# Performance work log

Hardware: AMD Instinct MI355X
Metric: run time of the kernel (lower is better)

The kernel has to match this reference:

```python
import jax, jax.numpy as jnp
import numpy as np

NUM_FEATURES = 35
NEG = -1e30  # effective -inf that is safe under exp/log


def setup_inputs() -> dict:
    key = jax.random.key(0)
    k1, k2, k3, k4 = jax.random.split(key, 4)
    B, T, S = 16, 500, 100
    logits = jax.random.normal(k1, (B, T, NUM_FEATURES), dtype=jnp.float32)
    targets = jax.random.randint(k2, (B, S, NUM_FEATURES), 0, 2, dtype=jnp.int32)
    input_lengths = jax.random.randint(k3, (B,), 300, T + 1, dtype=jnp.int32)
    target_lengths = jax.random.randint(k4, (B,), 10, S + 1, dtype=jnp.int32)
    blank_logit = jnp.zeros((1,), dtype=jnp.float32)
    return {"logits": logits, "blank_logit": blank_logit, "targets": targets,
            "input_lengths": input_lengths, "target_lengths": target_lengths}


def _lse3(a, b, c):
    m = jnp.maximum(jnp.maximum(a, b), c)
    return m + jnp.log(jnp.exp(a - m) + jnp.exp(b - m) + jnp.exp(c - m))


def _sctc_sb_loss(logits, blank_logit, targets, input_lengths, target_lengths):
    B, T, Fdim = logits.shape
    S = targets.shape[1]
    E = 2 * S + 1  # extended (blank-interleaved) target length

    # 3-class logits per feature: [absent=-x, present=x, shared blank]
    blank = jnp.broadcast_to(blank_logit.reshape(1, 1, 1), (B, T, Fdim))
    three = jnp.stack([-logits, logits, blank], axis=-1)           # (B,T,F,3)
    logp = jax.nn.log_softmax(three, axis=-1)                       # (B,T,F,3)

    # extended targets: [blank, y0, blank, y1, ..., blank], blank id = 2
    tgt = jnp.transpose(targets, (0, 2, 1))                         # (B,F,S)
    ext = jnp.full((B, Fdim, E), 2, dtype=jnp.int32)
    ext = ext.at[:, :, 1::2].set(tgt)                               # (B,F,E)

    # skip transition allowed if ext[s] != blank and ext[s] != ext[s-2]
    ext_m2 = jnp.pad(ext, ((0, 0), (0, 0), (2, 0)), constant_values=-1)[:, :, :E]
    allow_skip = (ext != 2) & (ext != ext_m2)                       # (B,F,E)

    # gather log-probs of extended labels: (T,B,F,E)
    lpT = jnp.transpose(logp, (1, 0, 2, 3))                         # (T,B,F,3)
    idx = jnp.broadcast_to(ext[None], (T, B, Fdim, E))
    lp_ext = jnp.take_along_axis(lpT, idx, axis=3)                  # (T,B,F,E)

    # alpha init at t=0
    alpha0 = jnp.full((B, Fdim, E), NEG, dtype=logp.dtype)
    alpha0 = alpha0.at[:, :, 0].set(lp_ext[0, :, :, 0])
    alpha0 = alpha0.at[:, :, 1].set(lp_ext[0, :, :, 1])

    def step(alpha, inp):
        lp_t, t = inp
        a1 = jnp.pad(alpha, ((0, 0), (0, 0), (1, 0)), constant_values=NEG)[:, :, :E]
        a2 = jnp.pad(alpha, ((0, 0), (0, 0), (2, 0)), constant_values=NEG)[:, :, :E]
        a2 = jnp.where(allow_skip, a2, NEG)
        new = _lse3(alpha, a1, a2) + lp_t
        active = (t < input_lengths)[:, None, None]
        return jnp.where(active, new, alpha), None

    alpha, _ = jax.lax.scan(step, alpha0, (lp_ext[1:], jnp.arange(1, T)))

    # log-likelihood = lse(alpha[2L], alpha[2L-1]) at final active frame
    L = target_lengths
    i1 = jnp.broadcast_to((2 * L)[:, None, None], (B, Fdim, 1))
    i2 = jnp.broadcast_to((2 * L - 1)[:, None, None], (B, Fdim, 1))
    aL = jnp.take_along_axis(alpha, i1, axis=2)[..., 0]
    aL1 = jnp.take_along_axis(alpha, i2, axis=2)[..., 0]
    m = jnp.maximum(aL, aL1)
    ll = m + jnp.log(jnp.exp(aL - m) + jnp.exp(aL1 - m))
    loss_bf = -ll                                                   # (B,F)
    # zero_infinity=True
    loss_bf = jnp.where(loss_bf > 0.5 * -NEG, 0.0, loss_bf)
    # CTCLoss reduction='mean': divide by target length, mean over batch;
    # then sum over features / NUM_FEATURES == mean over features
    per_bf = loss_bf / target_lengths[:, None].astype(loss_bf.dtype)
    return jnp.mean(per_bf)


def reference(logits, blank_logit, targets, input_lengths, target_lengths):
    return _sctc_sb_loss(logits, blank_logit, targets, input_lengths, target_lengths)
```

## Files before the change

kernel.cpp:

```cpp
#include <hip/hip_runtime.h>
#include <math.h>


#define LOG2E 1.4426950408889634f
#define LN2d 0.69314718055994530942

constexpr int Bc = 16, Tc = 500, Sc = 100, Fc = 35;
constexpr int NPAIR = Bc * Fc;
constexpr int EXPB = 217;

__device__ __forceinline__ float dpp_shr1(float v) {
  return __int_as_float(__builtin_amdgcn_update_dpp(
      0, __float_as_int(v), 0x138, 0xF, 0xF, false));
}
__device__ __forceinline__ float dpp_shl1(float v) {
  return __int_as_float(__builtin_amdgcn_update_dpp(
      0, __float_as_int(v), 0x130, 0xF, 0xF, false));
}
template <int C>
__device__ __forceinline__ int dppmax(int v) {
  int t = __builtin_amdgcn_update_dpp(v, v, C, 0xF, 0xF, false);
  return max(v, t);
}

__device__ __forceinline__ float4 smf(float xr, float bl2) {
  const float x = xr * LOG2E;
  const float m = fmaxf(fabsf(x), bl2);
  const float u0 = exp2f(-x - m), u1 = exp2f(x - m), u2 = exp2f(bl2 - m);
  const float rz = 1.0f / (u0 + u1 + u2);
  return make_float4(u2 * rz, u0 * rz, (u1 - u0) * rz, 0.0f);
}

template <bool BWD>
__device__ __forceinline__ void scan_dir(
    const float* __restrict__ lg, float bl2, int Tin, int L, int N,
    int tstart, float bt0f, float bt1f, float skXf, float skYf, int lane,
    float4 (*stg)[64], float& A0, float& A1, float& A2, float& A3,
    int& offOut) {
  float a0 = A0, a1 = A1, a2 = A2, a3 = A3;
  int off = -90;
  int mm = 0;

  const int e_hi = 2 * L + 1, twoLm1 = 2 * L - 1;
  const int e0 = 4 * lane;
  const bool in0 = e0 <= e_hi, in1 = e0 + 1 <= e_hi, in2 = e0 + 2 <= e_hi,
             in3 = e0 + 3 <= e_hi;

  auto addr = [&](int i) -> int {
    if (BWD) return max(tstart - i, 0);
    return min(tstart + i, Tc - 1);
  };

  auto step = [&](const float4& G) {
    const float po0 = fmaf(bt0f, G.z, G.y);
    const float po1 = fmaf(bt1f, G.z, G.y);
    if constexpr (!BWD) {
      const float pr3 = dpp_shr1(a3);
      const float s01 = a0 + a1, s12 = a1 + a2, s23 = a2 + a3;
      const float t0v = a0 + pr3;
      const float t1v = fmaf(pr3, skXf, s01);
      const float t3v = fmaf(a1, skYf, s23);
      a0 = t0v * G.x; a1 = t1v * po0; a2 = s12 * G.x; a3 = t3v * po1;
    } else {
      const float nb0 = dpp_shl1(a0);
      const float nb1 = dpp_shl1(a1);
      const float s01 = a0 + a1, s12 = a1 + a2, s23 = a2 + a3;
      const float t1v = fmaf(a3, skXf, s12);
      const float t3v = fmaf(nb1, skYf, a3 + nb0);
      a0 = s01 * G.x; a1 = t1v * po0; a2 = s23 * G.x; a3 = t3v * po1;
    }
  };

  auto snap = [&](int istep) {
    if constexpr (!BWD) {
      const int t = tstart + istep;
      const int elo = twoLm1 - 2 * (Tin - 1 - t);
      const int x0 = (in0 && e0 >= elo) ? (__float_as_int(a0) >> 23) : 0;
      const int x1 = (in1 && e0 + 1 >= elo) ? (__float_as_int(a1) >> 23) : 0;
      const int x2 = (in2 && e0 + 2 >= elo) ? (__float_as_int(a2) >> 23) : 0;
      const int x3 = (in3 && e0 + 3 >= elo) ? (__float_as_int(a3) >> 23) : 0;
      mm = max(max(x0, x1), max(x2, x3));
    } else {
      (void)istep;
      const int x0 = __float_as_int(a0) >> 23, x1 = __float_as_int(a1) >> 23;
      const int x2 = __float_as_int(a2) >> 23, x3 = __float_as_int(a3) >> 23;
      mm = max(max(x0, x1), max(x2, x3));
    }
  };
  auto tree = [&]() {
    mm = dppmax<0x111>(mm); mm = dppmax<0x112>(mm); mm = dppmax<0x114>(mm);
    mm = dppmax<0x118>(mm); mm = dppmax<0x142>(mm); mm = dppmax<0x143>(mm);
  };
  auto apply = [&]() {
    const int mw = __builtin_amdgcn_readlane(mm, 63);
    int k = EXPB - mw;
    k = min(max(k, -126), 126);
    const float sc = __int_as_float((k + 127) << 23);
    a0 *= sc; a1 *= sc; a2 *= sc; a3 *= sc;
    off -= k;
  };
  auto group = [&](float4 (&P)[8], float4 (&Q)[8], const float4* src,
                   int ilast) {
#pragma unroll
    for (int i = 0; i < 8; ++i) Q[i] = src[i];
    step(P[0]);
    tree();
    step(P[1]); step(P[2]); step(P[3]);
    apply();
    step(P[4]); step(P[5]); step(P[6]); step(P[7]);
    snap(ilast);
  };

  float xraw = lg[addr(lane) * Fc];
  stg[0][lane] = smf(xraw, bl2);
  xraw = lg[addr(64 + lane) * Fc];
  float4 A[8], B[8];
#pragma unroll
  for (int i = 0; i < 8; ++i) A[i] = stg[0][i];
  snap(-1);

  int buf = 0, ib = 0;
  for (; ib + 64 <= N; ib += 64) {
    if (ib + 64 < N) {
      stg[buf ^ 1][lane] = smf(xraw, bl2);
      xraw = lg[addr(ib + 128 + lane) * Fc];
    }
    const float4* cpA = &stg[buf][0];
    const float4* cpB = &stg[buf ^ 1][0];
#pragma unroll
    for (int d = 0; d < 4; ++d) {
      group(A, B, cpA + 8 * (2 * d + 1), ib + 16 * d + 7);
      group(B, A, (d < 3) ? (cpA + 8 * (2 * d + 2)) : cpB, ib + 16 * d + 15);
    }
    buf ^= 1;
  }
  {
    const int n = N - ib;
    const float4* cp = &stg[buf][0];
#pragma unroll
    for (int grp = 0; grp < 8; ++grp) {
      if (8 * grp >= n) break;
      float4 g[8];
#pragma unroll
      for (int i = 0; i < 8; ++i) g[i] = cp[8 * grp + i];
#pragma unroll
      for (int i = 0; i < 8; ++i) {
        if (8 * grp + i >= n) break;
        step(g[i]);
      }
      if (8 * grp + 8 <= n) { snap(ib + 8 * grp + 7); tree(); apply(); }
    }
  }
  A0 = a0; A1 = a1; A2 = a2; A3 = a3;
  offOut = off;
}

__global__ __launch_bounds__(128) void sctc_scan(
    const float* __restrict__ logits,
    const float* __restrict__ blank_logit,
    const int* __restrict__ targets,
    const int* __restrict__ in_len,
    const int* __restrict__ tgt_len,
    float* __restrict__ part) {
  __shared__ float4 stg[2][2][64];
  __shared__ float4 xch[64];
  __shared__ int offsh;
  const int tid = threadIdx.x, wid = tid >> 6, lane = tid & 63;
  const int p = blockIdx.x;
  const int b = p / Fc, f = p - b * Fc;
  const int Tin = in_len[b];
  const int L = tgt_len[b];
  const float bl2 = blank_logit[0] * LOG2E;
  const float* __restrict__ lg = logits + (size_t)b * Tc * Fc + f;
  const float S90 = __int_as_float((90 + 127) << 23);
  const int e0 = 4 * lane;

  const int tbase = b * Sc * Fc + f;
  const int t0 = targets[tbase + min(2 * lane, Sc - 1) * Fc];
  const int t1 = targets[tbase + min(2 * lane + 1, Sc - 1) * Fc];
  const int tprev = __shfl_up(t1, 1);
  const int tnext0 = __shfl_down(t0, 1);
  const float bt0f = t0 ? 1.0f : 0.0f, bt1f = t1 ? 1.0f : 0.0f;
  const float sk1f = (lane == 0 || t0 != tprev) ? 1.0f : 0.0f;
  const float sk3f = (t1 != t0) ? 1.0f : 0.0f;
  const float skBf = (tnext0 != t1) ? 1.0f : 0.0f;

  const int tm = Tin >> 1;
  const int NF = tm;
  const int NB = Tin - 2 - tm;

  float a0 = 0.0f, a1 = 0.0f, a2 = 0.0f, a3 = 0.0f;
  int off = -90;

  if (wid == 0) {
    const float4 c0 = smf(lg[0], bl2);
    if (lane == 0) {
      a0 = c0.x * S90;
      a1 = fmaf(bt0f, c0.z, c0.y) * S90;
    }
    scan_dir<false>(lg, bl2, Tin, L, NF, 1, bt0f, bt1f, sk1f, sk3f, lane,
                    stg[0], a0, a1, a2, a3, off);
  } else {
    const float4 cE = smf(lg[(Tin - 1) * Fc], bl2);
    if (e0 == 2 * L) a0 = cE.x * S90;
    if (e0 + 2 == 2 * L) a2 = cE.x * S90;
    if (e0 + 1 == 2 * L - 1) a1 = fmaf(bt0f, cE.z, cE.y) * S90;
    if (e0 + 3 == 2 * L - 1) a3 = fmaf(bt1f, cE.z, cE.y) * S90;
    scan_dir<true>(lg, bl2, Tin, L, NB, Tin - 2, bt0f, bt1f, sk3f, skBf,
                   lane, stg[1], a0, a1, a2, a3, off);
    const float nb0 = dpp_shl1(a0), nb1 = dpp_shl1(a1);
    const float bt0v = a0 + a1;
    const float bt1v = fmaf(a3, sk3f, a1 + a2);
    const float bt2v = a2 + a3;
    const float bt3v = fmaf(nb1, skBf, a3 + nb0);
    xch[lane] = make_float4(bt0v, bt1v, bt2v, bt3v);
    if (lane == 0) offsh = off;
  }
  __syncthreads();
  if (wid == 0) {
    const float4 bb = xch[lane];
    const int twoL = 2 * L;
    const float z0 = (e0 <= twoL) ? a0 : 0.0f;
    const float z1 = (e0 + 1 <= twoL) ? a1 : 0.0f;
    const float z2 = (e0 + 2 <= twoL) ? a2 : 0.0f;
    const float z3 = (e0 + 3 <= twoL) ? a3 : 0.0f;
    double d = (double)z0 * bb.x + (double)z1 * bb.y + (double)z2 * bb.z +
               (double)z3 * bb.w;
    for (int o = 32; o >= 1; o >>= 1) d += __shfl_down(d, o);
    if (lane == 0) {
      const int offT = off + offsh;
      float val = 0.0f;
      if (d > 0.0) {
        int ex;
        const double mant = frexp(d, &ex);
        const double ll2 = (double)(ex + offT) + log2(mant);
        double ld = -ll2 * LN2d;
        if (ld > 0.5e30) ld = 0.0;
        val = (float)(ld / (double)L) * (1.0f / (float)NPAIR);
      }
      part[p] = val;
    }
  }
}

__global__ __launch_bounds__(64) void sctc_reduce(const float* __restrict__ ws,
                                                  float* __restrict__ out) {
  const int lane = threadIdx.x;
  const float v0 = ws[lane];
  const float v1 = ws[lane + 64];
  const float v2 = ws[lane + 128];
  const float v3 = ws[lane + 192];
  const float v4 = ws[lane + 256];
  const float v5 = ws[lane + 320];
  const float v6 = ws[lane + 384];
  const float v7 = ws[lane + 448];
  float v8 = ws[(lane < 48) ? (lane + 512) : lane];
  if (lane >= 48) v8 = 0.0f;
  float s = ((((((((v0 + v1) + v2) + v3) + v4) + v5) + v6) + v7) + v8);
  for (int o = 32; o >= 1; o >>= 1) s += __shfl_xor(s, o);
  if (lane == 0) out[0] = s;
}

extern "C" void kernel_launch(void* const* d_in, const int* in_sizes, int n_in,
                              void* d_out, int out_size, void* d_ws,
                              size_t ws_size, hipStream_t stream) {
  const float* logits = (const float*)d_in[0];
  const float* blank_logit = (const float*)d_in[1];
  const int* targets = (const int*)d_in[2];
  const int* in_len = (const int*)d_in[3];
  const int* tgt_len = (const int*)d_in[4];
  float* part = (float*)d_ws;
  float* out = (float*)d_out;

  sctc_scan<<<NPAIR, 128, 0, stream>>>(logits, blank_logit, targets, in_len,
                                       tgt_len, part);
  sctc_reduce<<<1, 64, 0, stream>>>(part, out);
}
```

Baseline: 27.82 us.

## Fuse two CTC recurrence steps into one composed transition per iteration

Replaces pairs of single-timestep alpha/beta updates with a double step that applies the composed two-step transition matrix directly. Coefficients are built from both frames' probabilities, and neighbor values are fetched via DPP shifts of three or four registers. The aim is to halve the serial dependency chain of cross-lane shifts and dependent multiplies on the critical path. In exchange, each step does more ALU work, uses more registers, and needs extra per-lane neighbor target flags.

```diff
diff --git a/kernel.cpp b/kernel.cpp
--- a/kernel.cpp
+++ b/kernel.cpp
@@ -34,9 +34,9 @@
 template <bool BWD>
 __device__ __forceinline__ void scan_dir(
     const float* __restrict__ lg, float bl2, int Tin, int L, int N,
-    int tstart, float bt0f, float bt1f, float skXf, float skYf, int lane,
-    float4 (*stg)[64], float& A0, float& A1, float& A2, float& A3,
-    int& offOut) {
+    int tstart, float bt0f, float bt1f, float skXf, float skYf, float skNf,
+    float btNf, int lane, float4 (*stg)[64], float& A0, float& A1, float& A2,
+    float& A3, int& offOut) {
   float a0 = A0, a1 = A1, a2 = A2, a3 = A3;
   int off = -90;
   int mm = 0;
@@ -71,6 +71,79 @@
     }
   };
 
+  auto dstep = [&](const float4& GA, const float4& GB) {
+    const float q2a = GA.x, q0a = GA.y, qda = GA.z;
+    const float q2b = GB.x, q0b = GB.y, qdb = GB.z;
+    const float poXa = fmaf(bt0f, qda, q0a);
+    const float poYa = fmaf(bt1f, qda, q0a);
+    const float poNa = fmaf(btNf, qda, q0a);
+    const float poXb = fmaf(bt0f, qdb, q0b);
+    const float poYb = fmaf(bt1f, qdb, q0b);
+    if constexpr (!BWD) {
+      const float P3 = dpp_shr1(a3);
+      const float P2 = dpp_shr1(a2);
+      const float P1 = dpp_shr1(a1);
+      const float pNs = poNa * skNf;
+      const float C00 = q2b * q2a;
+      const float C0P3 = q2b * (q2a + poNa);
+      const float C0P2 = q2b * poNa;
+      const float C0P1 = q2b * pNs;
+      const float C11 = poXb * poXa;
+      const float C10 = poXb * (poXa + q2a);
+      const float C1P3 = poXb * fmaf(skXf, poXa + poNa, q2a);
+      const float s1pN = skXf * poNa;
+      const float C1P2 = poXb * s1pN;
+      const float C1P1 = poXb * (s1pN * skNf);
+      const float C21 = q2b * (q2a + poXa);
+      const float C20 = q2b * poXa;
+      const float C2P3 = C20 * skXf;
+      const float C33 = poYb * poYa;
+      const float C32 = poYb * (poYa + q2a);
+      const float C31 = poYb * fmaf(skYf, poYa + poXa, q2a);
+      const float s3pX = skYf * poXa;
+      const float C30 = poYb * s3pX;
+      const float C3P = poYb * (s3pX * skXf);
+      const float n0 = fmaf(C00, a0, C0P3 * P3) + fmaf(C0P2, P2, C0P1 * P1);
+      const float n1 = fmaf(C11, a1, C10 * a0) +
+                       fmaf(C1P3, P3, fmaf(C1P2, P2, C1P1 * P1));
+      const float n2 = fmaf(C00, a2, C21 * a1) + fmaf(C20, a0, C2P3 * P3);
+      const float n3 = fmaf(C33, a3, C32 * a2) +
+                       fmaf(C31, a1, fmaf(C30, a0, C3P * P3));
+      a0 = n0; a1 = n1; a2 = n2; a3 = n3;
+    } else {
+      const float N0 = dpp_shl1(a0);
+      const float N1 = dpp_shl1(a1);
+      const float N2 = dpp_shl1(a2);
+      const float N3 = dpp_shl1(a3);
+      const float D00 = q2b * q2a;
+      const float D01 = q2b * (q2a + poXa);
+      const float D02 = q2b * poXa;
+      const float D03 = D02 * skXf;
+      const float D11 = poXb * poXa;
+      const float D12 = poXb * (poXa + q2a);
+      const float D13 = poXb * fmaf(skXf, poXa + poYa, q2a);
+      const float s3Y = skXf * poYa;
+      const float D1N0 = poXb * s3Y;
+      const float D1N1 = poXb * (s3Y * skYf);
+      const float D23 = q2b * (q2a + poYa);
+      const float D2N0 = q2b * poYa;
+      const float D2N1 = D2N0 * skYf;
+      const float D33 = poYb * poYa;
+      const float D3N0 = poYb * (poYa + q2a);
+      const float D3N1 = poYb * fmaf(skYf, poYa + poNa, q2a);
+      const float w = skYf * poNa;
+      const float D3N2 = poYb * w;
+      const float D3N3 = poYb * (w * skNf);
+      const float n0 = fmaf(D00, a0, D01 * a1) + fmaf(D02, a2, D03 * a3);
+      const float n1 = fmaf(D11, a1, D12 * a2) +
+                       fmaf(D13, a3, fmaf(D1N0, N0, D1N1 * N1));
+      const float n2 = fmaf(D00, a2, D23 * a3) + fmaf(D2N0, N0, D2N1 * N1);
+      const float n3 = fmaf(D33, a3, D3N0 * N0) +
+                       fmaf(D3N1, N1, fmaf(D3N2, N2, D3N3 * N3));
+      a0 = n0; a1 = n1; a2 = n2; a3 = n3;
+    }
+  };
+
   auto snap = [&](int istep) {
     if constexpr (!BWD) {
       const int t = tstart + istep;
@@ -103,11 +176,12 @@
                    int ilast) {
 #pragma unroll
     for (int i = 0; i < 8; ++i) Q[i] = src[i];
-    step(P[0]);
+    dstep(P[0], P[1]);
     tree();
-    step(P[1]); step(P[2]); step(P[3]);
+    dstep(P[2], P[3]);
     apply();
-    step(P[4]); step(P[5]); step(P[6]); step(P[7]);
+    dstep(P[4], P[5]);
+    dstep(P[6], P[7]);
     snap(ilast);
   };
 
@@ -193,21 +267,25 @@
   int off = -90;
 
   if (wid == 0) {
+    const float skNf = __shfl_up(sk3f, 1);
+    const float btNf = __shfl_up(bt1f, 1);
     const float4 c0 = smf(lg[0], bl2);
     if (lane == 0) {
       a0 = c0.x * S90;
       a1 = fmaf(bt0f, c0.z, c0.y) * S90;
     }
-    scan_dir<false>(lg, bl2, Tin, L, NF, 1, bt0f, bt1f, sk1f, sk3f, lane,
-                    stg[0], a0, a1, a2, a3, off);
+    scan_dir<false>(lg, bl2, Tin, L, NF, 1, bt0f, bt1f, sk1f, sk3f, skNf,
+                    btNf, lane, stg[0], a0, a1, a2, a3, off);
   } else {
+    const float skNf = __shfl_down(sk3f, 1);
+    const float btNf = __shfl_down(bt0f, 1);
     const float4 cE = smf(lg[(Tin - 1) * Fc], bl2);
     if (e0 == 2 * L) a0 = cE.x * S90;
     if (e0 + 2 == 2 * L) a2 = cE.x * S90;
     if (e0 + 1 == 2 * L - 1) a1 = fmaf(bt0f, cE.z, cE.y) * S90;
     if (e0 + 3 == 2 * L - 1) a3 = fmaf(bt1f, cE.z, cE.y) * S90;
     scan_dir<true>(lg, bl2, Tin, L, NB, Tin - 2, bt0f, bt1f, sk3f, skBf,
-                   lane, stg[1], a0, a1, a2, a3, off);
+                   skNf, btNf, lane, stg[1], a0, a1, a2, a3, off);
     const float nb0 = dpp_shl1(a0), nb1 = dpp_shl1(a1);
     const float bt0v = a0 + a1;
     const float bt1v = fmaf(a3, sk3f, a1 + a2);
```

Result: slower. 37.56 us (+35.0%).
